# Kernel optimization log

Measured on AMD Instinct MI355X. Metric: run time of the kernel, lower is better.

The kernel has to match this reference:

```python
import jax, jax.numpy as jnp
import numpy as np
import math

ROPE_BASE = 10000.0

def rope(x):
    # rotate-half RoPE over the full feature dim. x: [B, S, D]
    B, S, D = x.shape
    half = D // 2
    inv_freq = 1.0 / (ROPE_BASE ** (jnp.arange(half, dtype=jnp.float32) / half))
    ang = jnp.arange(S, dtype=jnp.float32)[:, None] * inv_freq[None, :]  # [S, half]
    cos, sin = jnp.cos(ang), jnp.sin(ang)
    x1, x2 = x[..., :half], x[..., half:]
    return jnp.concatenate([x1 * cos - x2 * sin, x1 * sin + x2 * cos], axis=-1)

def setup_inputs() -> dict:
    key = jax.random.key(0)
    ks = jax.random.split(key, 10)
    B, S, D = 4, 2048, 2048
    scale = 1.0 / math.sqrt(D)
    x = jax.random.normal(ks[0], (B, S, D), dtype=jnp.float32)
    mask = jnp.broadcast_to(jnp.tril(jnp.ones((S, S), dtype=jnp.int32)), (B, S, S))
    Wq = jax.random.normal(ks[1], (D, D), dtype=jnp.float32) * scale
    bq = jax.random.normal(ks[2], (D,), dtype=jnp.float32) * 0.02
    Wk = jax.random.normal(ks[3], (D, D), dtype=jnp.float32) * scale
    bk = jax.random.normal(ks[4], (D,), dtype=jnp.float32) * 0.02
    Wv = jax.random.normal(ks[5], (D, D), dtype=jnp.float32) * scale
    bv = jax.random.normal(ks[6], (D,), dtype=jnp.float32) * 0.02
    Wo = jax.random.normal(ks[7], (D, D), dtype=jnp.float32) * scale
    bo = jax.random.normal(ks[8], (D,), dtype=jnp.float32) * 0.02
    return {"x": x, "mask": mask, "Wq": Wq, "bq": bq, "Wk": Wk, "bk": bk,
            "Wv": Wv, "bv": bv, "Wo": Wo, "bo": bo}

def reference(x, mask, Wq, bq, Wk, bk, Wv, bv, Wo, bo):
    # x: [B, S, D]; torch.nn.Linear convention: y = x @ W.T + b
    D = x.shape[-1]
    std = jnp.sqrt(jnp.asarray(D, dtype=x.dtype))
    q = jnp.einsum('bsd,ed->bse', x, Wq) + bq
    k = jnp.einsum('bsd,ed->bse', x, Wk) + bk
    v = jnp.einsum('bsd,ed->bse', x, Wv) + bv
    # cache=None prefill path: q sliced to last x.size(-2) positions (full seq here)
    Sq = x.shape[-2]
    q = rope(q)[:, -Sq:, :]
    k = rope(k)
    scores = jnp.einsum('bqd,bkd->bqk', q, k) / std  # [B, Sq, Sk]
    scores = jnp.where(mask[:, -Sq:, :] == 0, -jnp.inf, scores)
    attn = jax.nn.softmax(scores, axis=-1)  # dropout=0 (eval)
    ctx = jnp.einsum('bqk,bkd->bqd', attn, v)
    out = jnp.einsum('bqd,ed->bqe', ctx, Wo) + bo
    return out
```

## Files before the change

### kernel.cpp

```cpp
#include <hip/hip_runtime.h>
#include <stdint.h>
#include <math.h>

#define BLK 256

typedef __bf16 bf16x8 __attribute__((ext_vector_type(8)));
typedef float  f32x4  __attribute__((ext_vector_type(4)));

__device__ __forceinline__ uint16_t f2bf(float f) {
  uint32_t u = __float_as_uint(f);
  u += 0x7fffu + ((u >> 16) & 1u);
  return (uint16_t)(u >> 16);
}
__device__ __forceinline__ float bf2f(uint16_t h) {
  return __uint_as_float(((uint32_t)h) << 16);
}

__device__ __forceinline__ void load_lds16(const void* g, void* l) {
  __builtin_amdgcn_global_load_lds(
      (const __attribute__((address_space(1))) uint32_t*)g,
      (__attribute__((address_space(3))) uint32_t*)l,
      16, 0, 0);
}

__global__ __launch_bounds__(BLK)
void convert_all(const float* __restrict__ x, const float* __restrict__ wq,
                 const float* __restrict__ wk, const float* __restrict__ wv,
                 const float* __restrict__ wo,
                 uint16_t* __restrict__ xb, uint16_t* __restrict__ wqkv) {
  const long XG = 4194304;
  const long T  = XG + 4 * 1048576;
  for (long i = (long)blockIdx.x * BLK + threadIdx.x; i < T; i += (long)gridDim.x * BLK) {
    const float* src; uint16_t* dst; long off;
    if (i < XG) { src = x; dst = xb; off = i; }
    else {
      const long j = i - XG;
      const int seg = (int)(j >> 20);
      off = j & 1048575;
      src = (seg == 0) ? wq : (seg == 1) ? wk : (seg == 2) ? wv : wo;
      dst = wqkv + ((long)seg << 22);
    }
    float4 v = ((const float4*)src)[off];
    ushort4 o;
    o.x = f2bf(v.x); o.y = f2bf(v.y); o.z = f2bf(v.z); o.w = f2bf(v.w);
    ((ushort4*)dst)[off] = o;
  }
}

template<bool OUT_BF16, bool TRI_GRID, bool K_TRI, int MINW>
__global__ __launch_bounds__(BLK, MINW)
void gemm_bt(const uint16_t* __restrict__ A, int lda,
             const uint16_t* __restrict__ Bt, int ldb,
             const float* __restrict__ b0, const float* __restrict__ b1,
             const float* __restrict__ b2,
             void* __restrict__ Cv, int ldc,
             int M, int N, int K,
             long sAb, long sBb, long sCb,
             float scale, float* __restrict__ rowsum)
{
  int tile_m, tile_n, bz;
  if (TRI_GRID) {
    const int t = blockIdx.x;
    int r = (int)((sqrtf(8.f * (float)t + 1.f) - 1.f) * 0.5f);
    while ((r + 1) * (r + 2) / 2 <= t) ++r;
    while (r * (r + 1) / 2 > t) --r;
    tile_m = r * 128;
    tile_n = (t - r * (r + 1) / 2) * 128;
    bz = blockIdx.z;
  } else if (K_TRI) {
    bz = blockIdx.y & 3;
    tile_m = ((int)(gridDim.y >> 2) - 1 - (int)(blockIdx.y >> 2)) * 128;
    tile_n = blockIdx.x * 128;
  } else {
    tile_m = blockIdx.y * 128;
    tile_n = blockIdx.x * 128;
    bz = blockIdx.z;
  }
  A  += (long)bz * sAb;
  Bt += (long)bz * sBb;

  __shared__ __align__(16) uint16_t sA[128 * 64];
  __shared__ __align__(16) uint16_t sB[128 * 64];

  const int tid  = threadIdx.x;
  const int lane = tid & 63;
  const int wave = tid >> 6;
  const int quad = lane >> 4;
  const int l16  = lane & 15;
  const int x8   = l16 & 7;
  const int wm = (wave & 1) * 64;
  const int wn = (wave >> 1) * 64;

  f32x4 acc[4][4];
#pragma unroll
  for (int i = 0; i < 4; ++i)
#pragma unroll
    for (int j = 0; j < 4; ++j) acc[i][j] = (f32x4){0.f, 0.f, 0.f, 0.f};

  const uint16_t* gA[4]; const uint16_t* gB[4];
  uint16_t* lA[4]; uint16_t* lB[4];
#pragma unroll
  for (int i = 0; i < 4; ++i) {
    const int id = wave * 256 + i * 64 + lane;
    const int row = id >> 3;
    const int c = (id & 7) ^ (row & 7);
    gA[i] = A  + (long)(tile_m + row) * lda + c * 8;
    gB[i] = Bt + (long)(tile_n + row) * ldb + c * 8;
    lA[i] = sA + (wave * 256 + i * 64) * 8;
    lB[i] = sB + (wave * 256 + i * 64) * 8;
  }

  const int kend = K_TRI ? min(K, tile_m + 128) : K;

  for (int kk = 0; kk < kend; kk += 64) {
#pragma unroll
    for (int i = 0; i < 4; ++i) {
      load_lds16(gA[i] + kk, lA[i]);
      load_lds16(gB[i] + kk, lB[i]);
    }
    __syncthreads();

#pragma unroll
    for (int s2 = 0; s2 < 2; ++s2) {
      const int slot = ((quad + s2 * 4) ^ x8) * 8;
      bf16x8 af[4], bfr[4];
#pragma unroll
      for (int mi = 0; mi < 4; ++mi)
        af[mi] = *(const bf16x8*)(sA + (wm + mi * 16 + l16) * 64 + slot);
#pragma unroll
      for (int ni = 0; ni < 4; ++ni)
        bfr[ni] = *(const bf16x8*)(sB + (wn + ni * 16 + l16) * 64 + slot);
#pragma unroll
      for (int mi = 0; mi < 4; ++mi)
#pragma unroll
        for (int ni = 0; ni < 4; ++ni)
          acc[mi][ni] = __builtin_amdgcn_mfma_f32_16x16x32_bf16(af[mi], bfr[ni], acc[mi][ni], 0, 0, 0);
    }
    __syncthreads();
  }

  const int crow0 = tile_m + wm + quad * 4;
  const int ccol0 = tile_n + wn + l16;

  if constexpr (TRI_GRID) {
    const bool diag = (tile_m == tile_n);
    uint16_t* Pp = (uint16_t*)Cv + (long)bz * sCb;
    float* rs = rowsum + (long)bz * 2048;
#pragma unroll
    for (int mi = 0; mi < 4; ++mi) {
#pragma unroll
      for (int r = 0; r < 4; ++r) {
        const int row = crow0 + mi * 16 + r;
        float partial = 0.f;
#pragma unroll
        for (int ni = 0; ni < 4; ++ni) {
          const int col = ccol0 + ni * 16;
          const float e = (!diag || col <= row) ? __expf(acc[mi][ni][r] * scale) : 0.f;
          const uint16_t h = f2bf(e);
          partial += bf2f(h);
          Pp[(long)row * ldc + col] = h;
        }
#pragma unroll
        for (int o = 1; o < 16; o <<= 1) partial += __shfl_xor(partial, o, 64);
        if (l16 == 0) atomicAdd(rs + row, partial);
      }
    }
  } else if constexpr (K_TRI) {
    uint16_t* Cp = (uint16_t*)Cv + (long)bz * sCb;
    const float* rs = rowsum + (long)bz * 2048;
#pragma unroll
    for (int mi = 0; mi < 4; ++mi) {
#pragma unroll
      for (int r = 0; r < 4; ++r) {
        const int row = crow0 + mi * 16 + r;
        const float inv = 1.f / rs[row];
#pragma unroll
        for (int ni = 0; ni < 4; ++ni)
          Cp[(long)row * ldc + ccol0 + ni * 16] = f2bf(acc[mi][ni][r] * inv);
      }
    }
  } else {
    const int seg = tile_n >> 11;
    const float* bp = (seg == 0) ? b0 : ((seg == 1) ? b1 : b2);
#pragma unroll
    for (int ni = 0; ni < 4; ++ni) {
      const int col = ccol0 + ni * 16;
      const float bb = bp ? bp[col & 2047] : 0.f;
#pragma unroll
      for (int mi = 0; mi < 4; ++mi) {
#pragma unroll
        for (int r = 0; r < 4; ++r) {
          const long row = crow0 + mi * 16 + r;
          const float v = acc[mi][ni][r] * scale + bb;
          if (OUT_BF16)
            ((uint16_t*)Cv + (long)bz * sCb)[row * (long)ldc + col] = f2bf(v);
          else
            ((float*)Cv + (long)bz * sCb)[row * (long)ldc + col] = v;
        }
      }
    }
  }
}

__global__ __launch_bounds__(BLK)
void rope_kernel(uint16_t* __restrict__ QKV) {
  const long idx = (long)blockIdx.x * BLK + threadIdx.x;
  const long t = idx >> 8;
  const int  i4 = (int)(idx & 255) << 2;
  const int  s = (int)(t & 2047);
  uint16_t* base = QKV + t * 6144;

  float cs[4], sn[4];
#pragma unroll
  for (int j = 0; j < 4; ++j) {
    const float invf = exp2f((float)(i4 + j) * (-13.287712379549449f / 1024.f));
    __sincosf((float)s * invf, &sn[j], &cs[j]);
  }
#pragma unroll
  for (int seg = 0; seg < 2; ++seg) {
    uint16_t* p = base + seg * 2048 + i4;
    ushort4 a = *(ushort4*)p;
    ushort4 b = *(ushort4*)(p + 1024);
    ushort4 oa, ob;
    const uint16_t* ap = (const uint16_t*)&a;
    const uint16_t* bpp = (const uint16_t*)&b;
    uint16_t* oap = (uint16_t*)&oa;
    uint16_t* obp = (uint16_t*)&ob;
#pragma unroll
    for (int j = 0; j < 4; ++j) {
      const float x1 = bf2f(ap[j]), x2 = bf2f(bpp[j]);
      oap[j] = f2bf(x1 * cs[j] - x2 * sn[j]);
      obp[j] = f2bf(x1 * sn[j] + x2 * cs[j]);
    }
    *(ushort4*)p = oa;
    *(ushort4*)(p + 1024) = ob;
  }
}

__global__ __launch_bounds__(BLK)
void transpose_v(const uint16_t* __restrict__ in , uint16_t* __restrict__ out) {
  const long bz = blockIdx.z;
  __shared__ uint16_t tile[32][33];
  const int tx = threadIdx.x & 31, ty = threadIdx.x >> 5;
  const int bx = blockIdx.x * 32;
  const int by = blockIdx.y * 32;
#pragma unroll
  for (int r = ty; r < 32; r += 8)
    tile[r][tx] = in[(bz * 2048 + by + r) * 6144 + bx + tx];
  __syncthreads();
  uint16_t* o = out + bz * 4194304;
#pragma unroll
  for (int r = ty; r < 32; r += 8)
    o[(long)(bx + r) * 2048 + by + tx] = tile[tx][r];
}

extern "C" void kernel_launch(void* const* d_in, const int* in_sizes, int n_in,
                              void* d_out, int out_size, void* d_ws, size_t ws_size,
                              hipStream_t stream) {
  const long S = 2048, D = 2048;
  const long MD = 4 * S * D;
  const long DD = D * D;

  const float* x  = (const float*)d_in[0];
  const float* Wq = (const float*)d_in[2];
  const float* bq = (const float*)d_in[3];
  const float* Wk = (const float*)d_in[4];
  const float* bk = (const float*)d_in[5];
  const float* Wv = (const float*)d_in[6];
  const float* bv = (const float*)d_in[7];
  const float* Wo = (const float*)d_in[8];
  const float* bo = (const float*)d_in[9];

  uint16_t* Xb    = (uint16_t*)d_ws;
  uint16_t* Wqkvb = Xb + MD;
  uint16_t* QKV   = Wqkvb + 4 * DD;
  uint16_t* Vt    = QKV + 8192L * 6144;
  uint16_t* P     = Vt + MD;
  float*    sums  = (float*)(P + 4 * S * S);
  if (ws_size < 268435456ull) return;

  dim3 blk(BLK);

  hipMemsetAsync(sums, 0, 8192 * sizeof(float), stream);

  convert_all<<<16384, blk, 0, stream>>>(x, Wq, Wk, Wv, Wo, Xb, Wqkvb);

  gemm_bt<true, false, false, 4><<<dim3(48, 64, 1), blk, 0, stream>>>(
      Xb, 2048, Wqkvb, 2048, bq, bk, bv, QKV, 6144, 8192, 6144, 2048,
      0, 0, 0, 1.f, nullptr);

  rope_kernel<<<8192, blk, 0, stream>>>(QKV);

  transpose_v<<<dim3(64, 64, 4), blk, 0, stream>>>(QKV + 4096, Vt);

  gemm_bt<true, true, false, 3><<<dim3(136, 1, 4), blk, 0, stream>>>(
      QKV, 6144, QKV + 2048, 6144, nullptr, nullptr, nullptr, P, 2048,
      2048, 2048, 2048, 2048L * 6144, 2048L * 6144, S * S,
      0.022097086912079608f, sums);

  gemm_bt<true, false, true, 4><<<dim3(16, 64, 1), blk, 0, stream>>>(
      P, 2048, Vt, 2048, nullptr, nullptr, nullptr, Xb, 2048,
      2048, 2048, 2048, S * S, S * D, S * D, 1.f, sums);

  gemm_bt<false, false, false, 4><<<dim3(16, 64, 1), blk, 0, stream>>>(
      Xb, 2048, Wqkvb + 3 * DD, 2048, bo, bo, bo, (float*)d_out, 2048,
      8192, 2048, 2048, 0, 0, 0, 1.f, nullptr);
}
```

Before: 624.3 us.

## Fuse RoPE and V transpose into QKV GEMM epilogue via interleaved weight rows

Wq and Wk rows are permuted during bf16 conversion so each rotate-half pair lands in adjacent columns. The QKV GEMM epilogue can then apply RoPE with a lane shuffle, and it writes V transposed through shared memory. This removes the separate rope and transpose kernels and their extra global round trips. The sums memset is folded into the convert kernel. Costs: per-element sincos in the GEMM epilogue, an extra LDS pass for V, and a lower occupancy hint on the QKV GEMM.

```diff
diff --git a/kernel.cpp b/kernel.cpp
--- a/kernel.cpp
+++ b/kernel.cpp
@@ -27,39 +27,48 @@
 void convert_all(const float* __restrict__ x, const float* __restrict__ wq,
                  const float* __restrict__ wk, const float* __restrict__ wv,
                  const float* __restrict__ wo,
-                 uint16_t* __restrict__ xb, uint16_t* __restrict__ wqkv) {
+                 uint16_t* __restrict__ xb, uint16_t* __restrict__ wqkv,
+                 float* __restrict__ sums) {
+  const long tid0 = (long)blockIdx.x * BLK + threadIdx.x;
+  if (tid0 < 8192) sums[tid0] = 0.f;
   const long XG = 4194304;
   const long T  = XG + 4 * 1048576;
-  for (long i = (long)blockIdx.x * BLK + threadIdx.x; i < T; i += (long)gridDim.x * BLK) {
-    const float* src; uint16_t* dst; long off;
-    if (i < XG) { src = x; dst = xb; off = i; }
+  for (long i = tid0; i < T; i += (long)gridDim.x * BLK) {
+    const float* src; uint16_t* dst; long off, doff;
+    if (i < XG) { src = x; dst = xb; off = i; doff = i; }
     else {
       const long j = i - XG;
       const int seg = (int)(j >> 20);
       off = j & 1048575;
       src = (seg == 0) ? wq : (seg == 1) ? wk : (seg == 2) ? wv : wo;
       dst = wqkv + ((long)seg << 22);
+      if (seg < 2) {
+        const int f = (int)(off >> 9);
+        const int g = (int)(off & 511);
+        const int c = (f < 1024) ? (f << 1) : (((f - 1024) << 1) | 1);
+        doff = (long)c * 512 + g;
+      } else doff = off;
     }
     float4 v = ((const float4*)src)[off];
     ushort4 o;
     o.x = f2bf(v.x); o.y = f2bf(v.y); o.z = f2bf(v.z); o.w = f2bf(v.w);
-    ((ushort4*)dst)[off] = o;
-  }
-}
-
-template<bool OUT_BF16, bool TRI_GRID, bool K_TRI, int MINW>
+    ((ushort4*)dst)[doff] = o;
+  }
+}
+
+template<int MODE, int MINW>
 __global__ __launch_bounds__(BLK, MINW)
 void gemm_bt(const uint16_t* __restrict__ A, int lda,
              const uint16_t* __restrict__ Bt, int ldb,
              const float* __restrict__ b0, const float* __restrict__ b1,
              const float* __restrict__ b2,
              void* __restrict__ Cv, int ldc,
-             int M, int N, int K,
-             long sAb, long sBb, long sCb,
-             float scale, float* __restrict__ rowsum)
+             int K, long sAb, long sBb, long sCb,
+             float scale, float* __restrict__ rowsum,
+             uint16_t* __restrict__ Vt)
 {
   int tile_m, tile_n, bz;
-  if (TRI_GRID) {
+  if (MODE == 2) {
     const int t = blockIdx.x;
     int r = (int)((sqrtf(8.f * (float)t + 1.f) - 1.f) * 0.5f);
     while ((r + 1) * (r + 2) / 2 <= t) ++r;
@@ -67,7 +76,7 @@
     tile_m = r * 128;
     tile_n = (t - r * (r + 1) / 2) * 128;
     bz = blockIdx.z;
-  } else if (K_TRI) {
+  } else if (MODE == 3) {
     bz = blockIdx.y & 3;
     tile_m = ((int)(gridDim.y >> 2) - 1 - (int)(blockIdx.y >> 2)) * 128;
     tile_n = blockIdx.x * 128;
@@ -79,8 +88,9 @@
   A  += (long)bz * sAb;
   Bt += (long)bz * sBb;
 
-  __shared__ __align__(16) uint16_t sA[128 * 64];
-  __shared__ __align__(16) uint16_t sB[128 * 64];
+  __shared__ __align__(16) uint16_t smem[16384];
+  uint16_t* sA = smem;
+  uint16_t* sB = smem + 8192;
 
   const int tid  = threadIdx.x;
   const int lane = tid & 63;
@@ -110,7 +120,7 @@
     lB[i] = sB + (wave * 256 + i * 64) * 8;
   }
 
-  const int kend = K_TRI ? min(K, tile_m + 128) : K;
+  const int kend = (MODE == 3) ? min(K, tile_m + 128) : K;
 
   for (int kk = 0; kk < kend; kk += 64) {
 #pragma unroll
@@ -142,7 +152,7 @@
   const int crow0 = tile_m + wm + quad * 4;
   const int ccol0 = tile_n + wn + l16;
 
-  if constexpr (TRI_GRID) {
+  if constexpr (MODE == 2) {
     const bool diag = (tile_m == tile_n);
     uint16_t* Pp = (uint16_t*)Cv + (long)bz * sCb;
     float* rs = rowsum + (long)bz * 2048;
@@ -165,7 +175,7 @@
         if (l16 == 0) atomicAdd(rs + row, partial);
       }
     }
-  } else if constexpr (K_TRI) {
+  } else if constexpr (MODE == 3) {
     uint16_t* Cp = (uint16_t*)Cv + (long)bz * sCb;
     const float* rs = rowsum + (long)bz * 2048;
 #pragma unroll
@@ -179,79 +189,75 @@
           Cp[(long)row * ldc + ccol0 + ni * 16] = f2bf(acc[mi][ni][r] * inv);
       }
     }
+  } else if constexpr (MODE == 1) {
+    const int seg = tile_n >> 11;
+    if (seg < 2) {
+      const float* bp = seg ? b1 : b0;
+      uint16_t* Cp = (uint16_t*)Cv;
+#pragma unroll
+      for (int ni = 0; ni < 4; ++ni) {
+        const int col = ccol0 + ni * 16;
+        const int cc = col & 2047;
+        const float bb = bp[(cc >> 1) + (cc & 1) * 1024];
+        const float invf = exp2f((float)(cc >> 1) * (-13.287712379549449f / 1024.f));
+        const float sgn = (cc & 1) ? 1.f : -1.f;
+#pragma unroll
+        for (int mi = 0; mi < 4; ++mi) {
+#pragma unroll
+          for (int r = 0; r < 4; ++r) {
+            const int row = crow0 + mi * 16 + r;
+            const float v = acc[mi][ni][r] + bb;
+            float sn, cs;
+            __sincosf((float)(row & 2047) * invf, &sn, &cs);
+            const float p = __shfl_xor(v, 1, 64);
+            Cp[(long)row * 4096 + col] = f2bf(v * cs + p * sgn * sn);
+          }
+        }
+      }
+    } else {
+#pragma unroll
+      for (int ni = 0; ni < 4; ++ni) {
+        const int cl = wn + l16 + ni * 16;
+        const float bb = b2[(ccol0 + ni * 16) & 2047];
+#pragma unroll
+        for (int mi = 0; mi < 4; ++mi) {
+          const int rl0 = wm + quad * 4 + mi * 16;
+          union { uint16_t u16[4]; uint64_t u64; } pk;
+#pragma unroll
+          for (int r = 0; r < 4; ++r) pk.u16[r] = f2bf(acc[mi][ni][r] + bb);
+          *(uint64_t*)(smem + cl * 128 + (rl0 ^ ((cl & 15) << 3))) = pk.u64;
+        }
+      }
+      __syncthreads();
+      const int fl = quad;
+      const int t0 = l16 * 8;
+      const int bno = tile_m >> 11;
+      const int tokbase = tile_m & 2047;
+      uint16_t* Vp = Vt + (long)bno * 4194304 + tokbase;
+      const int featbase = tile_n - 4096;
+#pragma unroll
+      for (int jj = 0; jj < 8; ++jj) {
+        const int c = jj * 16 + wave * 4 + fl;
+        const uint16_t* srcp = smem + c * 128 + (t0 ^ ((c & 15) << 3));
+        ulonglong2 v = *(const ulonglong2*)srcp;
+        *(ulonglong2*)(Vp + (long)(featbase + c) * 2048 + t0) = v;
+      }
+    }
   } else {
-    const int seg = tile_n >> 11;
-    const float* bp = (seg == 0) ? b0 : ((seg == 1) ? b1 : b2);
 #pragma unroll
     for (int ni = 0; ni < 4; ++ni) {
       const int col = ccol0 + ni * 16;
-      const float bb = bp ? bp[col & 2047] : 0.f;
+      const float bb = b0[col];
 #pragma unroll
       for (int mi = 0; mi < 4; ++mi) {
 #pragma unroll
         for (int r = 0; r < 4; ++r) {
           const long row = crow0 + mi * 16 + r;
-          const float v = acc[mi][ni][r] * scale + bb;
-          if (OUT_BF16)
-            ((uint16_t*)Cv + (long)bz * sCb)[row * (long)ldc + col] = f2bf(v);
-          else
-            ((float*)Cv + (long)bz * sCb)[row * (long)ldc + col] = v;
+          ((float*)Cv)[row * (long)ldc + col] = acc[mi][ni][r] * scale + bb;
         }
       }
     }
   }
-}
-
-__global__ __launch_bounds__(BLK)
-void rope_kernel(uint16_t* __restrict__ QKV) {
-  const long idx = (long)blockIdx.x * BLK + threadIdx.x;
-  const long t = idx >> 8;
-  const int  i4 = (int)(idx & 255) << 2;
-  const int  s = (int)(t & 2047);
-  uint16_t* base = QKV + t * 6144;
-
-  float cs[4], sn[4];
-#pragma unroll
-  for (int j = 0; j < 4; ++j) {
-    const float invf = exp2f((float)(i4 + j) * (-13.287712379549449f / 1024.f));
-    __sincosf((float)s * invf, &sn[j], &cs[j]);
-  }
-#pragma unroll
-  for (int seg = 0; seg < 2; ++seg) {
-    uint16_t* p = base + seg * 2048 + i4;
-    ushort4 a = *(ushort4*)p;
-    ushort4 b = *(ushort4*)(p + 1024);
-    ushort4 oa, ob;
-    const uint16_t* ap = (const uint16_t*)&a;
-    const uint16_t* bpp = (const uint16_t*)&b;
-    uint16_t* oap = (uint16_t*)&oa;
-    uint16_t* obp = (uint16_t*)&ob;
-#pragma unroll
-    for (int j = 0; j < 4; ++j) {
-      const float x1 = bf2f(ap[j]), x2 = bf2f(bpp[j]);
-      oap[j] = f2bf(x1 * cs[j] - x2 * sn[j]);
-      obp[j] = f2bf(x1 * sn[j] + x2 * cs[j]);
-    }
-    *(ushort4*)p = oa;
-    *(ushort4*)(p + 1024) = ob;
-  }
-}
-
-__global__ __launch_bounds__(BLK)
-void transpose_v(const uint16_t* __restrict__ in , uint16_t* __restrict__ out) {
-  const long bz = blockIdx.z;
-  __shared__ uint16_t tile[32][33];
-  const int tx = threadIdx.x & 31, ty = threadIdx.x >> 5;
-  const int bx = blockIdx.x * 32;
-  const int by = blockIdx.y * 32;
-#pragma unroll
-  for (int r = ty; r < 32; r += 8)
-    tile[r][tx] = in[(bz * 2048 + by + r) * 6144 + bx + tx];
-  __syncthreads();
-  uint16_t* o = out + bz * 4194304;
-#pragma unroll
-  for (int r = ty; r < 32; r += 8)
-    o[(long)(bx + r) * 2048 + by + tx] = tile[tx][r];
 }
 
 extern "C" void kernel_launch(void* const* d_in, const int* in_sizes, int n_in,
@@ -273,36 +279,30 @@
 
   uint16_t* Xb    = (uint16_t*)d_ws;
   uint16_t* Wqkvb = Xb + MD;
-  uint16_t* QKV   = Wqkvb + 4 * DD;
-  uint16_t* Vt    = QKV + 8192L * 6144;
+  uint16_t* QK    = Wqkvb + 4 * DD;
+  uint16_t* Vt    = QK + 8192L * 4096;
   uint16_t* P     = Vt + MD;
   float*    sums  = (float*)(P + 4 * S * S);
   if (ws_size < 268435456ull) return;
 
   dim3 blk(BLK);
 
-  hipMemsetAsync(sums, 0, 8192 * sizeof(float), stream);
-
-  convert_all<<<16384, blk, 0, stream>>>(x, Wq, Wk, Wv, Wo, Xb, Wqkvb);
-
-  gemm_bt<true, false, false, 4><<<dim3(48, 64, 1), blk, 0, stream>>>(
-      Xb, 2048, Wqkvb, 2048, bq, bk, bv, QKV, 6144, 8192, 6144, 2048,
-      0, 0, 0, 1.f, nullptr);
-
-  rope_kernel<<<8192, blk, 0, stream>>>(QKV);
-
-  transpose_v<<<dim3(64, 64, 4), blk, 0, stream>>>(QKV + 4096, Vt);
-
-  gemm_bt<true, true, false, 3><<<dim3(136, 1, 4), blk, 0, stream>>>(
-      QKV, 6144, QKV + 2048, 6144, nullptr, nullptr, nullptr, P, 2048,
-      2048, 2048, 2048, 2048L * 6144, 2048L * 6144, S * S,
-      0.022097086912079608f, sums);
-
-  gemm_bt<true, false, true, 4><<<dim3(16, 64, 1), blk, 0, stream>>>(
+  convert_all<<<16384, blk, 0, stream>>>(x, Wq, Wk, Wv, Wo, Xb, Wqkvb, sums);
+
+  gemm_bt<1, 3><<<dim3(48, 64, 1), blk, 0, stream>>>(
+      Xb, 2048, Wqkvb, 2048, bq, bk, bv, QK, 4096,
+      2048, 0, 0, 0, 1.f, nullptr, Vt);
+
+  gemm_bt<2, 3><<<dim3(136, 1, 4), blk, 0, stream>>>(
+      QK, 4096, QK + 2048, 4096, nullptr, nullptr, nullptr, P, 2048,
+      2048, 2048L * 4096, 2048L * 4096, S * S,
+      0.022097086912079608f, sums, nullptr);
+
+  gemm_bt<3, 4><<<dim3(16, 64, 1), blk, 0, stream>>>(
       P, 2048, Vt, 2048, nullptr, nullptr, nullptr, Xb, 2048,
-      2048, 2048, 2048, S * S, S * D, S * D, 1.f, sums);
-
-  gemm_bt<false, false, false, 4><<<dim3(16, 64, 1), blk, 0, stream>>>(
-      Xb, 2048, Wqkvb + 3 * DD, 2048, bo, bo, bo, (float*)d_out, 2048,
-      8192, 2048, 2048, 0, 0, 0, 1.f, nullptr);
-}
+      2048, S * S, S * D, S * D, 1.f, sums, nullptr);
+
+  gemm_bt<0, 4><<<dim3(16, 64, 1), blk, 0, stream>>>(
+      Xb, 2048, Wqkvb + 3 * DD, 2048, bo, nullptr, nullptr, (float*)d_out, 2048,
+      2048, 0, 0, 0, 1.f, nullptr, nullptr);
+}
```

Result: faster. 586.3 us (-6.1%).
